# Optimization experiments

Hardware: AMD Instinct MI355X
Metric: run time of the kernel (lower is better)

Reference implementation:

```python
import jax, jax.numpy as jnp
import numpy as np

BL = 512
Q_DIM = K_DIM = V_DIM = 512
R = 2
C = Q_DIM // R  # 256


def setup_inputs() -> dict:
    key = jax.random.key(0)
    ks = jax.random.split(key, 11)
    L = 32768
    x1 = jax.random.normal(ks[0], (1, Q_DIM, L), dtype=jnp.float32)
    x2 = jax.random.normal(ks[1], (1, Q_DIM, L), dtype=jnp.float32)
    mask = jnp.ones((1, 1, L), dtype=jnp.float32)
    s_in = 1.0 / np.sqrt(Q_DIM)
    s_out = 1.0 / np.sqrt(C)
    Wq = jax.random.normal(ks[2], (C, Q_DIM), dtype=jnp.float32) * s_in
    bq = jax.random.normal(ks[3], (C,), dtype=jnp.float32) * 0.01
    Wk = jax.random.normal(ks[4], (C, K_DIM), dtype=jnp.float32) * s_in
    bk = jax.random.normal(ks[5], (C,), dtype=jnp.float32) * 0.01
    Wv = jax.random.normal(ks[6], (C, V_DIM), dtype=jnp.float32) * s_in
    bv = jax.random.normal(ks[7], (C,), dtype=jnp.float32) * 0.01
    Wo = jax.random.normal(ks[8], (V_DIM, C), dtype=jnp.float32) * s_out
    bo = jax.random.normal(ks[9], (V_DIM,), dtype=jnp.float32) * 0.01
    return {"x1": x1, "x2": x2, "mask": mask, "Wq": Wq, "bq": bq,
            "Wk": Wk, "bk": bk, "Wv": Wv, "bv": bv, "Wo": Wo, "bo": bo}


def _sliding_att(x1, mask, Wq, bq, Wk, bk, Wv, bv, Wo, bo):
    bl = BL
    half = bl // 2
    B, _, L = x1.shape  # B == 1 (asserted in original)
    # 1x1 Conv1d projections == per-position matmuls over channels
    q = jnp.einsum('oc,bcl->bol', Wq, x1) + bq[None, :, None]  # (1,C,L)
    k = jnp.einsum('oc,bcl->bol', Wk, x1) + bk[None, :, None]
    v = jnp.einsum('oc,bcl->bol', Wv, x1) + bv[None, :, None]
    c1 = q.shape[1]
    nb = L // bl  # L chosen as multiple of bl; padding branch is a no-op
    pm = mask[:, 0:1, :]  # (1,1,L)
    # query blocks: (nb, C, bl)
    qb = q.reshape(1, c1, nb, bl).transpose(0, 2, 1, 3).reshape(nb, c1, bl)
    # pad K/V/mask with bl//2 zeros each side, gather overlapping windows of width 2*bl
    k_pad = jnp.pad(k, ((0, 0), (0, 0), (half, half)))[0]      # (C, L+bl)
    v_pad = jnp.pad(v, ((0, 0), (0, 0), (half, half)))[0]
    pm_pad = jnp.pad(pm, ((0, 0), (0, 0), (half, half)))[0, 0]  # (L+bl,)
    idx = jnp.arange(nb)[:, None] * bl + jnp.arange(2 * bl)[None, :]  # (nb, 2bl)
    kw = k_pad[:, idx].transpose(1, 0, 2)  # (nb, C, 2bl)
    vw = v_pad[:, idx].transpose(1, 0, 2)  # (nb, C, 2bl)
    pmw = pm_pad[idx][:, None, :]          # (nb, 1, 2bl)
    # banded window mask: query i attends keys j with i <= j < i+bl (in window coords)
    rows = jnp.arange(bl)[:, None]
    cols = jnp.arange(2 * bl)[None, :]
    wmask = ((cols >= rows) & (cols < rows + bl)).astype(x1.dtype)  # (bl, 2bl)
    fmask = wmask[None, :, :] * pmw  # (nb, bl, 2bl)
    scale = 1.0 / np.sqrt(c1)
    energy = jnp.einsum('ncl,ncm->nlm', qb, kw) * scale  # (nb, bl, 2bl)
    attn = jax.nn.softmax(energy + jnp.log(fmask + 1e-6), axis=-1) * fmask
    out = jnp.einsum('ncm,nlm->ncl', vw, attn)  # (nb, C, bl)
    out = jax.nn.relu(out)
    out = jnp.einsum('oc,ncl->nol', Wo, out) + bo[None, :, None]  # (nb, V, bl)
    out = out[None].transpose(0, 2, 1, 3).reshape(1, Wo.shape[0], nb * bl)
    return out[:, :, :L] * pm


def reference(x1, x2, mask, Wq, bq, Wk, bk, Wv, bv, Wo, bo):
    # x2 is accepted by the original forward but unused in self-attention
    return _sliding_att(x1, mask, Wq, bq, Wk, bk, Wv, bv, Wo, bo)
```

## Files before the change

kernel.cpp:

```cpp
#include <hip/hip_runtime.h>
#include <hip/hip_bf16.h>
#include <math.h>

#define L 32768
#define C 256
#define QD 512
#define SCALE (1.0f/16.0f)

typedef __hip_bfloat16 bf16;
typedef short v8s __attribute__((ext_vector_type(8)));
typedef short v4s __attribute__((ext_vector_type(4)));
typedef float v4f __attribute__((ext_vector_type(4)));

__device__ __forceinline__ void ldst16(void* lds, const void* g) {
    __builtin_amdgcn_global_load_lds(
        (const __attribute__((address_space(1))) unsigned int*)g,
        (__attribute__((address_space(3))) unsigned int*)lds, 16, 0, 0);
}
__device__ __forceinline__ short bfbits(float x) {
    bf16 h = __float2bfloat16(x);
    return *reinterpret_cast<short*>(&h);
}

__global__ __launch_bounds__(256) void prep(
    const float* __restrict__ Wq, const float* __restrict__ Wk,
    const float* __restrict__ Wv, const float* __restrict__ bq,
    const float* __restrict__ bk, const float* __restrict__ bv,
    const float* __restrict__ Wo,
    bf16* __restrict__ Wall, bf16* __restrict__ Wob, float* __restrict__ ball)
{
    int i = blockIdx.x * 256 + threadIdx.x;
    if (i < 768*512) {
        int row = i >> 9, idx = i & 511;
        const float* src = row < 256 ? Wq : row < 512 ? Wk : Wv;
        Wall[i] = __float2bfloat16(src[(row & 255) * 512 + idx]);
    } else if (i < 768*512 + 512*256) {
        int j = i - 768*512;
        Wob[j] = __float2bfloat16(Wo[j]);
    } else if (i < 768*512 + 512*256 + 768) {
        int j = i - 768*512 - 512*256;
        ball[j] = j < 256 ? bq[j] : j < 512 ? bk[j - 256] : bv[j - 512];
    }
}

__global__ __launch_bounds__(256) void convt(
    const float* __restrict__ x, short* __restrict__ xT)
{
    __shared__ short st[64*72];
    const int t = threadIdx.x;
    const int l0 = blockIdx.x * 64, c0 = blockIdx.y * 64;
    #pragma unroll
    for (int i = 0; i < 2; i++) {
        int v = i*256 + t;
        int c = v >> 3, l8 = (v & 7) << 3;
        const float* p = x + (size_t)(c0 + c) * L + l0 + l8;
        float4 f0 = *(const float4*)p;
        float4 f1 = *(const float4*)(p + 4);
        bf16* stb = (bf16*)st;
        stb[(l8+0)*72 + c] = __float2bfloat16(f0.x);
        stb[(l8+1)*72 + c] = __float2bfloat16(f0.y);
        stb[(l8+2)*72 + c] = __float2bfloat16(f0.z);
        stb[(l8+3)*72 + c] = __float2bfloat16(f0.w);
        stb[(l8+4)*72 + c] = __float2bfloat16(f1.x);
        stb[(l8+5)*72 + c] = __float2bfloat16(f1.y);
        stb[(l8+6)*72 + c] = __float2bfloat16(f1.z);
        stb[(l8+7)*72 + c] = __float2bfloat16(f1.w);
    }
    __syncthreads();
    #pragma unroll
    for (int i = 0; i < 2; i++) {
        int v = i*256 + t;
        int l = v >> 3, c8 = (v & 7) << 3;
        *(v8s*)(xT + (size_t)(l0 + l) * QD + c0 + c8) = *(const v8s*)&st[l*72 + c8];
    }
}

__global__ __launch_bounds__(256) void qkv_gemm(
    const bf16* __restrict__ A, const bf16* __restrict__ B,
    const float* __restrict__ ball,
    bf16* __restrict__ qT, bf16* __restrict__ kT, bf16* __restrict__ vB)
{
    __shared__ short sA[128*32];
    __shared__ short sB[128*32];
    __shared__ short sE[128*136];

    const int t    = threadIdx.x;
    const int lane = t & 63;
    const int w    = t >> 6;
    const int wm   = w & 1, wn = w >> 1;
    const int col  = lane & 15, quad = lane >> 4;
    const int n0   = blockIdx.x * 128;
    const int my   = blockIdx.y;
    const int m0   = my * 128;

    v4f acc[4][4];
    #pragma unroll
    for (int i = 0; i < 4; i++)
        #pragma unroll
        for (int j = 0; j < 4; j++) acc[i][j] = (v4f){0.f,0.f,0.f,0.f};

    for (int k0 = 0; k0 < QD; k0 += 32) {
        #pragma unroll
        for (int j = 0; j < 2; j++) {
            int idx = j*256 + t;
            int m = idx >> 2, k8 = (idx & 3) << 3;
            ldst16(&sA[idx*8], A + (size_t)(m0 + m) * QD + k0 + k8);
        }
        #pragma unroll
        for (int j = 0; j < 2; j++) {
            int idx = j*256 + t;
            int n = idx >> 2, k8 = (idx & 3) << 3;
            ldst16(&sB[idx*8], B + (size_t)(n0 + n) * QD + k0 + k8);
        }
        __syncthreads();
        v8s af[4], bf[4];
        #pragma unroll
        for (int mt = 0; mt < 4; mt++)
            af[mt] = *(const v8s*)&sA[(wm*64 + mt*16 + col)*32 + quad*8];
        #pragma unroll
        for (int nt = 0; nt < 4; nt++)
            bf[nt] = *(const v8s*)&sB[(wn*64 + nt*16 + col)*32 + quad*8];
        #pragma unroll
        for (int mt = 0; mt < 4; mt++)
            #pragma unroll
            for (int nt = 0; nt < 4; nt++)
                acc[mt][nt] = __builtin_amdgcn_mfma_f32_16x16x32_bf16(af[mt], bf[nt], acc[mt][nt], 0, 0, 0);
        __syncthreads();
    }

    float bias_v[4][4];
    #pragma unroll
    for (int mt = 0; mt < 4; mt++)
        #pragma unroll
        for (int r = 0; r < 4; r++)
            bias_v[mt][r] = ball[m0 + wm*64 + mt*16 + quad*4 + r];

    bf16* sEb = (bf16*)sE;
    if (my < 4) {
        #pragma unroll
        for (int mt = 0; mt < 4; mt++)
            #pragma unroll
            for (int nt = 0; nt < 4; nt++)
                #pragma unroll
                for (int r = 0; r < 4; r++)
                    sEb[(wn*64 + nt*16 + col)*136 + wm*64 + mt*16 + quad*4 + r] =
                        __float2bfloat16(acc[mt][nt][r] + bias_v[mt][r]);
        __syncthreads();
        bf16* dst = (my < 2) ? qT : kT;
        const int c0 = (my & 1) * 128;
        #pragma unroll
        for (int j = 0; j < 8; j++) {
            int idx = j*256 + t;
            int n = idx >> 4, c8 = (idx & 15) << 3;
            *(v8s*)(dst + (size_t)(n0 + n) * C + c0 + c8) = *(const v8s*)&sE[n*136 + c8];
        }
    } else {
        #pragma unroll
        for (int mt = 0; mt < 4; mt++)
            #pragma unroll
            for (int nt = 0; nt < 4; nt++)
                #pragma unroll
                for (int r = 0; r < 4; r++)
                    sEb[(wm*64 + mt*16 + quad*4 + r)*136 + wn*64 + nt*16 + col] =
                        __float2bfloat16(acc[mt][nt][r] + bias_v[mt][r]);
        __syncthreads();
        const int c0 = (my - 4) * 128;
        #pragma unroll
        for (int j = 0; j < 8; j++) {
            int idx = j*256 + t;
            int m = idx >> 4, n8 = (idx & 15) << 3;
            *(v8s*)(vB + (size_t)(c0 + m) * L + n0 + n8) = *(const v8s*)&sE[m*136 + n8];
        }
    }
}

__global__ __launch_bounds__(256) void out_gemm(
    const bf16* __restrict__ A, const bf16* __restrict__ B,
    const float* __restrict__ bo, const float* __restrict__ mask,
    float* __restrict__ out)
{
    __shared__ short sA[128*32];
    __shared__ short sB[128*32];

    const int t    = threadIdx.x;
    const int lane = t & 63;
    const int w    = t >> 6;
    const int wm   = w & 1, wn = w >> 1;
    const int col  = lane & 15, quad = lane >> 4;
    const int n0   = blockIdx.x * 128;
    const int m0   = blockIdx.y * 128;

    v4f acc[4][4];
    #pragma unroll
    for (int i = 0; i < 4; i++)
        #pragma unroll
        for (int j = 0; j < 4; j++) acc[i][j] = (v4f){0.f,0.f,0.f,0.f};

    for (int k0 = 0; k0 < C; k0 += 32) {
        #pragma unroll
        for (int j = 0; j < 2; j++) {
            int idx = j*256 + t;
            int m = idx >> 2, k8 = (idx & 3) << 3;
            ldst16(&sA[idx*8], A + (size_t)(m0 + m) * C + k0 + k8);
        }
        #pragma unroll
        for (int j = 0; j < 2; j++) {
            int idx = j*256 + t;
            int n = idx >> 2, k8 = (idx & 3) << 3;
            ldst16(&sB[idx*8], B + (size_t)(n0 + n) * C + k0 + k8);
        }
        __syncthreads();
        v8s af[4], bf[4];
        #pragma unroll
        for (int mt = 0; mt < 4; mt++)
            af[mt] = *(const v8s*)&sA[(wm*64 + mt*16 + col)*32 + quad*8];
        #pragma unroll
        for (int nt = 0; nt < 4; nt++)
            bf[nt] = *(const v8s*)&sB[(wn*64 + nt*16 + col)*32 + quad*8];
        #pragma unroll
        for (int mt = 0; mt < 4; mt++)
            #pragma unroll
            for (int nt = 0; nt < 4; nt++)
                acc[mt][nt] = __builtin_amdgcn_mfma_f32_16x16x32_bf16(af[mt], bf[nt], acc[mt][nt], 0, 0, 0);
        __syncthreads();
    }

    float bias_v[4];
    #pragma unroll
    for (int mt = 0; mt < 4; mt++)
        bias_v[mt] = 0.f;
    #pragma unroll
    for (int mt = 0; mt < 4; mt++) {
        #pragma unroll
        for (int r = 0; r < 4; r++) {
            int m = m0 + wm*64 + mt*16 + quad*4 + r;
            float bb = bo[m];
            #pragma unroll
            for (int nt = 0; nt < 4; nt++) {
                int n = n0 + wn*64 + nt*16 + col;
                out[(size_t)m * L + n] = (acc[mt][nt][r] + bb) * mask[n];
            }
        }
    }
}

__global__ __launch_bounds__(256, 2) void attn_mfma(
    const bf16* __restrict__ qT, const bf16* __restrict__ kT,
    const bf16* __restrict__ vB, const float* __restrict__ mask,
    bf16* __restrict__ aoT)
{
    __shared__ short sK [64*264];
    __shared__ short sVt[256*72];
    __shared__ short sP [4][16*72];

    const int t    = threadIdx.x;
    const int w    = t >> 6;
    const int lane = t & 63;
    const int col  = lane & 15;
    const int quad = lane >> 4;
    const int p0   = blockIdx.x * 64;
    const int abase = p0 - 256;

    v8s qf[8];
    {
        const short* qp = (const short*)qT + (size_t)(p0 + w*16 + col) * C + quad*8;
        #pragma unroll
        for (int ks = 0; ks < 8; ks++) qf[ks] = *(const v8s*)(qp + ks*32);
    }

    v4f oacc[16];
    #pragma unroll
    for (int i = 0; i < 16; i++) oacc[i] = (v4f){0.f, 0.f, 0.f, 0.f};
    float mrow[4] = {-1e30f, -1e30f, -1e30f, -1e30f};
    float lrow[4] = {0.f, 0.f, 0.f, 0.f};

    for (int ch = 0; ch < 9; ch++) {
        const int a0 = abase + ch*64;
        __syncthreads();
        #pragma unroll
        for (int i = 0; i < 8; i++) {
            int idx = i*256 + t;
            int r = idx >> 5, cb = (idx & 31) << 3;
            int a = a0 + r;
            v8s val = {0,0,0,0,0,0,0,0};
            if (a >= 0 && a < L)
                val = *(const v8s*)((const short*)kT + (size_t)a * C + cb);
            *(v8s*)&sK[r*264 + cb] = val;
        }
        if (a0 >= 0 && a0 + 63 < L) {
            #pragma unroll
            for (int i = 0; i < 8; i++) {
                int idx = i*256 + t;
                int c = idx >> 3, kb = (idx & 7) << 3;
                *(v8s*)&sVt[c*72 + kb] =
                    *(const v8s*)((const short*)vB + (size_t)c * L + a0 + kb);
            }
        } else {
            #pragma unroll
            for (int i = 0; i < 8; i++) {
                int idx = i*256 + t;
                int c = idx >> 3, kb = (idx & 7) << 3;
                v8s val;
                #pragma unroll
                for (int j = 0; j < 8; j++) {
                    int a = a0 + kb + j;
                    val[j] = (a >= 0 && a < L)
                        ? ((const short*)vB)[(size_t)c * L + a] : (short)0;
                }
                *(v8s*)&sVt[c*72 + kb] = val;
            }
        }
        __syncthreads();

        v4f e[4];
        #pragma unroll
        for (int nt = 0; nt < 4; nt++) {
            v4f acc = {0.f, 0.f, 0.f, 0.f};
            const short* kp = &sK[(nt*16 + col)*264 + quad*8];
            #pragma unroll
            for (int ks = 0; ks < 8; ks++) {
                v8s bfrag = *(const v8s*)(kp + ks*32);
                acc = __builtin_amdgcn_mfma_f32_16x16x32_bf16(qf[ks], bfrag, acc, 0, 0, 0);
            }
            e[nt] = acc;
        }

        float cmax[4] = {-1e30f, -1e30f, -1e30f, -1e30f};
        #pragma unroll
        for (int nt = 0; nt < 4; nt++) {
            int a  = a0 + nt*16 + col;
            int aa = ch*64 + nt*16 + col;
            float mval = (a >= 0 && a < L) ? mask[a] : 0.f;
            #pragma unroll
            for (int r = 0; r < 4; r++) {
                int rel = aa - (w*16 + quad*4 + r);
                bool valid = ((unsigned)rel < 512u) && (mval > 0.f);
                float ev = valid ? e[nt][r] * SCALE : -1e30f;
                e[nt][r] = ev;
                cmax[r] = fmaxf(cmax[r], ev);
            }
        }
        #pragma unroll
        for (int off = 1; off < 16; off <<= 1) {
            #pragma unroll
            for (int r = 0; r < 4; r++)
                cmax[r] = fmaxf(cmax[r], __shfl_xor(cmax[r], off));
        }

        float alpha[4];
        #pragma unroll
        for (int r = 0; r < 4; r++) {
            float mnew = fmaxf(mrow[r], cmax[r]);
            alpha[r] = __expf(mrow[r] - mnew);
            mrow[r] = mnew;
        }

        float psum[4] = {0.f, 0.f, 0.f, 0.f};
        bf16* sPw = (bf16*)sP[w];
        #pragma unroll
        for (int nt = 0; nt < 4; nt++) {
            #pragma unroll
            for (int r = 0; r < 4; r++) {
                float ev = e[nt][r];
                float p = (ev > -9e29f) ? __expf(ev - mrow[r]) : 0.f;
                psum[r] += p;
                sPw[(quad*4 + r)*72 + nt*16 + col] = __float2bfloat16(p);
            }
        }
        #pragma unroll
        for (int off = 1; off < 16; off <<= 1) {
            #pragma unroll
            for (int r = 0; r < 4; r++)
                psum[r] += __shfl_xor(psum[r], off);
        }
        #pragma unroll
        for (int r = 0; r < 4; r++) lrow[r] = lrow[r]*alpha[r] + psum[r];

        {
            int src = (col >> 2) << 4;
            float a0b = __shfl(alpha[0], src);
            float a1b = __shfl(alpha[1], src);
            float a2b = __shfl(alpha[2], src);
            float a3b = __shfl(alpha[3], src);
            int rr = col & 3;
            float aO = (rr == 0) ? a0b : (rr == 1) ? a1b : (rr == 2) ? a2b : a3b;
            #pragma unroll
            for (int i = 0; i < 16; i++) {
                oacc[i][0] *= aO; oacc[i][1] *= aO;
                oacc[i][2] *= aO; oacc[i][3] *= aO;
            }
        }

        {
            const short* sPws = (const short*)sP[w];
            v8s pf0 = *(const v8s*)&sPws[col*72 + quad*8];
            v8s pf1 = *(const v8s*)&sPws[col*72 + quad*8 + 32];
            #pragma unroll
            for (int ct = 0; ct < 16; ct++) {
                const short* vp = &sVt[(ct*16 + col)*72 + quad*8];
                v8s vf0 = *(const v8s*)vp;
                v8s vf1 = *(const v8s*)(vp + 32);
                oacc[ct] = __builtin_amdgcn_mfma_f32_16x16x32_bf16(vf0, pf0, oacc[ct], 0, 0, 0);
                oacc[ct] = __builtin_amdgcn_mfma_f32_16x16x32_bf16(vf1, pf1, oacc[ct], 0, 0, 0);
            }
        }
    }

    {
        int src = (col >> 2) << 4;
        float l0b = __shfl(lrow[0], src);
        float l1b = __shfl(lrow[1], src);
        float l2b = __shfl(lrow[2], src);
        float l3b = __shfl(lrow[3], src);
        int rr = col & 3;
        float lO = (rr == 0) ? l0b : (rr == 1) ? l1b : (rr == 2) ? l2b : l3b;
        float inv = (lO > 0.f) ? 1.f / lO : 0.f;
        const int qg = p0 + w*16 + col;
        short* aorow = (short*)aoT + (size_t)qg * C;
        #pragma unroll
        for (int ct = 0; ct < 16; ct++) {
            v4s pk;
            #pragma unroll
            for (int r = 0; r < 4; r++)
                pk[r] = bfbits(fmaxf(oacc[ct][r] * inv, 0.f));
            *(v4s*)(aorow + ct*16 + quad*4) = pk;
        }
    }
}

extern "C" void kernel_launch(void* const* d_in, const int* in_sizes, int n_in,
                              void* d_out, int out_size, void* d_ws, size_t ws_size,
                              hipStream_t stream)
{
    const float* x1   = (const float*)d_in[0];
    const float* mask = (const float*)d_in[2];
    const float* Wq   = (const float*)d_in[3];
    const float* bq   = (const float*)d_in[4];
    const float* Wk   = (const float*)d_in[5];
    const float* bk   = (const float*)d_in[6];
    const float* Wv   = (const float*)d_in[7];
    const float* bv   = (const float*)d_in[8];
    const float* Wo   = (const float*)d_in[9];
    const float* bo   = (const float*)d_in[10];
    float* out = (float*)d_out;

    bf16* x1T  = (bf16*)d_ws;
    bf16* Wall = x1T + (size_t)L * QD;
    bf16* Wob  = Wall + 768*512;
    float* ball = (float*)(Wob + 512*256);
    bf16* qT   = (bf16*)(ball + 768);
    bf16* kT   = qT + (size_t)L * C;
    bf16* vB   = kT + (size_t)L * C;
    bf16* aoT  = vB + (size_t)L * C;

    dim3 blk(256);
    prep<<<dim3((768*512 + 512*256 + 768 + 255)/256), blk, 0, stream>>>(
        Wq, Wk, Wv, bq, bk, bv, Wo, Wall, Wob, ball);
    convt<<<dim3(L/64, QD/64), blk, 0, stream>>>(x1, (short*)x1T);
    qkv_gemm<<<dim3(L/128, 6), blk, 0, stream>>>(Wall, x1T, ball, qT, kT, vB);
    attn_mfma<<<dim3(L/64), blk, 0, stream>>>(qT, kT, vB, mask, aoT);
    out_gemm<<<dim3(L/128, 4), blk, 0, stream>>>(Wob, aoT, bo, mask, out);
}
```

Measured before the change: 304.5 us.

## Double-buffer K/V loads via registers, widen attention tile, coalesce output stores

The attention kernel now uses 512 threads covering 128 queries per block, so each streamed K/V chunk serves twice as many queries and there are fewer redundant window loads (10 chunks per 128 queries instead of 9 per 64). The next chunk is prefetched into registers while the current one is computed, then written to LDS, which hides global load latency. Block indices are swizzled to change tile ordering. The output GEMM epilogue stages results through shared memory to emit coalesced float4 stores with vectorized mask loads. The costs are extra register pressure from the prefetch buffers and extra LDS use and barriers in out_gemm.

```diff
diff --git a/kernel.cpp b/kernel.cpp
--- a/kernel.cpp
+++ b/kernel.cpp
@@ -181,6 +181,7 @@
 {
     __shared__ short sA[128*32];
     __shared__ short sB[128*32];
+    __shared__ float sEf[64*132];
 
     const int t    = threadIdx.x;
     const int lane = t & 63;
@@ -225,40 +226,106 @@
         __syncthreads();
     }
 
-    float bias_v[4];
-    #pragma unroll
-    for (int mt = 0; mt < 4; mt++)
-        bias_v[mt] = 0.f;
-    #pragma unroll
-    for (int mt = 0; mt < 4; mt++) {
-        #pragma unroll
-        for (int r = 0; r < 4; r++) {
-            int m = m0 + wm*64 + mt*16 + quad*4 + r;
-            float bb = bo[m];
-            #pragma unroll
-            for (int nt = 0; nt < 4; nt++) {
-                int n = n0 + wn*64 + nt*16 + col;
-                out[(size_t)m * L + n] = (acc[mt][nt][r] + bb) * mask[n];
-            }
-        }
-    }
-}
-
-__global__ __launch_bounds__(256, 2) void attn_mfma(
+    #pragma unroll
+    for (int half = 0; half < 2; half++) {
+        if (wm == half) {
+            #pragma unroll
+            for (int mt = 0; mt < 4; mt++) {
+                #pragma unroll
+                for (int r = 0; r < 4; r++) {
+                    float bb = bo[m0 + half*64 + mt*16 + quad*4 + r];
+                    #pragma unroll
+                    for (int nt = 0; nt < 4; nt++)
+                        sEf[(mt*16 + quad*4 + r)*132 + wn*64 + nt*16 + col] =
+                            acc[mt][nt][r] + bb;
+                }
+            }
+        }
+        __syncthreads();
+        #pragma unroll
+        for (int j = 0; j < 8; j++) {
+            int idx = j*256 + t;
+            int row = idx >> 5, s4 = (idx & 31) << 2;
+            float4 vv = *(const float4*)&sEf[row*132 + s4];
+            float4 mk = *(const float4*)&mask[n0 + s4];
+            vv.x *= mk.x; vv.y *= mk.y; vv.z *= mk.z; vv.w *= mk.w;
+            *(float4*)&out[(size_t)(m0 + half*64 + row) * L + n0 + s4] = vv;
+        }
+        __syncthreads();
+    }
+}
+
+__device__ __forceinline__ void load_chunk(
+    const short* __restrict__ kT, const short* __restrict__ vB,
+    int a0, int t, v8s kreg[4], v8s vreg[4])
+{
+    #pragma unroll
+    for (int j = 0; j < 4; j++) {
+        int idx = j*512 + t;
+        int r = idx >> 5, s = idx & 31;
+        int a = a0 + r;
+        v8s kv = {0,0,0,0,0,0,0,0};
+        if (a >= 0 && a < L) kv = *(const v8s*)(kT + (size_t)a * C + s*8);
+        kreg[j] = kv;
+    }
+    if (a0 >= 0 && a0 + 63 < L) {
+        #pragma unroll
+        for (int j = 0; j < 4; j++) {
+            int idx = j*512 + t;
+            int c = idx >> 3, s = idx & 7;
+            vreg[j] = *(const v8s*)(vB + (size_t)c * L + a0 + s*8);
+        }
+    } else {
+        #pragma unroll
+        for (int j = 0; j < 4; j++) {
+            int idx = j*512 + t;
+            int c = idx >> 3, s = idx & 7;
+            v8s val;
+            #pragma unroll
+            for (int e2 = 0; e2 < 8; e2++) {
+                int a = a0 + s*8 + e2;
+                val[e2] = (a >= 0 && a < L) ? vB[(size_t)c * L + a] : (short)0;
+            }
+            vreg[j] = val;
+        }
+    }
+}
+
+__device__ __forceinline__ void store_chunk(
+    short* __restrict__ sK, short* __restrict__ sVt, int t,
+    const v8s kreg[4], const v8s vreg[4])
+{
+    #pragma unroll
+    for (int j = 0; j < 4; j++) {
+        int idx = j*512 + t;
+        int r = idx >> 5, s = idx & 31;
+        *(v8s*)&sK[r*264 + s*8] = kreg[j];
+    }
+    #pragma unroll
+    for (int j = 0; j < 4; j++) {
+        int idx = j*512 + t;
+        int c = idx >> 3, s = idx & 7;
+        *(v8s*)&sVt[c*72 + s*8] = vreg[j];
+    }
+}
+
+__global__ __launch_bounds__(512, 2) void attn_mfma(
     const bf16* __restrict__ qT, const bf16* __restrict__ kT,
     const bf16* __restrict__ vB, const float* __restrict__ mask,
     bf16* __restrict__ aoT)
 {
     __shared__ short sK [64*264];
     __shared__ short sVt[256*72];
-    __shared__ short sP [4][16*72];
+    __shared__ short sP [8][16*72];
 
     const int t    = threadIdx.x;
     const int w    = t >> 6;
     const int lane = t & 63;
     const int col  = lane & 15;
     const int quad = lane >> 4;
-    const int p0   = blockIdx.x * 64;
+    const int bx   = blockIdx.x;
+    const int tile = ((bx & 7) << 5) | (bx >> 3);
+    const int p0   = tile * 128;
     const int abase = p0 - 256;
 
     v8s qf[8];
@@ -274,43 +341,16 @@
     float mrow[4] = {-1e30f, -1e30f, -1e30f, -1e30f};
     float lrow[4] = {0.f, 0.f, 0.f, 0.f};
 
-    for (int ch = 0; ch < 9; ch++) {
+    v8s kreg[4], vreg[4];
+    load_chunk((const short*)kT, (const short*)vB, abase, t, kreg, vreg);
+    store_chunk(sK, sVt, t, kreg, vreg);
+    __syncthreads();
+
+    for (int ch = 0; ch < 10; ch++) {
         const int a0 = abase + ch*64;
-        __syncthreads();
-        #pragma unroll
-        for (int i = 0; i < 8; i++) {
-            int idx = i*256 + t;
-            int r = idx >> 5, cb = (idx & 31) << 3;
-            int a = a0 + r;
-            v8s val = {0,0,0,0,0,0,0,0};
-            if (a >= 0 && a < L)
-                val = *(const v8s*)((const short*)kT + (size_t)a * C + cb);
-            *(v8s*)&sK[r*264 + cb] = val;
-        }
-        if (a0 >= 0 && a0 + 63 < L) {
-            #pragma unroll
-            for (int i = 0; i < 8; i++) {
-                int idx = i*256 + t;
-                int c = idx >> 3, kb = (idx & 7) << 3;
-                *(v8s*)&sVt[c*72 + kb] =
-                    *(const v8s*)((const short*)vB + (size_t)c * L + a0 + kb);
-            }
-        } else {
-            #pragma unroll
-            for (int i = 0; i < 8; i++) {
-                int idx = i*256 + t;
-                int c = idx >> 3, kb = (idx & 7) << 3;
-                v8s val;
-                #pragma unroll
-                for (int j = 0; j < 8; j++) {
-                    int a = a0 + kb + j;
-                    val[j] = (a >= 0 && a < L)
-                        ? ((const short*)vB)[(size_t)c * L + a] : (short)0;
-                }
-                *(v8s*)&sVt[c*72 + kb] = val;
-            }
-        }
-        __syncthreads();
+        const bool pf = (ch < 9);
+        if (pf)
+            load_chunk((const short*)kT, (const short*)vB, a0 + 64, t, kreg, vreg);
 
         v4f e[4];
         #pragma unroll
@@ -403,6 +443,12 @@
                 oacc[ct] = __builtin_amdgcn_mfma_f32_16x16x32_bf16(vf0, pf0, oacc[ct], 0, 0, 0);
                 oacc[ct] = __builtin_amdgcn_mfma_f32_16x16x32_bf16(vf1, pf1, oacc[ct], 0, 0, 0);
             }
+        }
+
+        if (pf) {
+            __syncthreads();
+            store_chunk(sK, sVt, t, kreg, vreg);
+            __syncthreads();
         }
     }
 
@@ -458,6 +504,6 @@
         Wq, Wk, Wv, bq, bk, bv, Wo, Wall, Wob, ball);
     convt<<<dim3(L/64, QD/64), blk, 0, stream>>>(x1, (short*)x1T);
     qkv_gemm<<<dim3(L/128, 6), blk, 0, stream>>>(Wall, x1T, ball, qT, kT, vB);
-    attn_mfma<<<dim3(L/64), blk, 0, stream>>>(qT, kT, vB, mask, aoT);
+    attn_mfma<<<dim3(L/128), dim3(512), 0, stream>>>(qT, kT, vB, mask, aoT);
     out_gemm<<<dim3(L/128, 4), blk, 0, stream>>>(Wob, aoT, bo, mask, out);
 }
```

New measurement: 292.0 us. 1.04x faster.

## Load K/V fragments directly from global in attention and stage output GEMM stores through LDS

Applied to the files above, without the earlier changes.

The attention kernel stops staging K and V chunks in shared memory. Each wave now reads MFMA fragments straight from global memory, with clamped indices so boundary rows stay in bounds and masking handles validity. This removes two block barriers per chunk and raises the occupancy hint to 3, and block indices are remapped so neighbouring tiles run apart. The output GEMM epilogue writes results into an LDS buffer and then emits coalesced float4 stores with the mask applied. The cost is redundant global and L2 traffic, since all four waves fetch the same K/V data.

```diff
diff --git a/kernel.cpp b/kernel.cpp
--- a/kernel.cpp
+++ b/kernel.cpp
@@ -181,6 +181,7 @@
 {
     __shared__ short sA[128*32];
     __shared__ short sB[128*32];
+    __shared__ float sEf[64*132];
 
     const int t    = threadIdx.x;
     const int lane = t & 63;
@@ -225,40 +226,50 @@
         __syncthreads();
     }
 
-    float bias_v[4];
-    #pragma unroll
-    for (int mt = 0; mt < 4; mt++)
-        bias_v[mt] = 0.f;
-    #pragma unroll
-    for (int mt = 0; mt < 4; mt++) {
-        #pragma unroll
-        for (int r = 0; r < 4; r++) {
-            int m = m0 + wm*64 + mt*16 + quad*4 + r;
-            float bb = bo[m];
-            #pragma unroll
-            for (int nt = 0; nt < 4; nt++) {
-                int n = n0 + wn*64 + nt*16 + col;
-                out[(size_t)m * L + n] = (acc[mt][nt][r] + bb) * mask[n];
-            }
-        }
-    }
-}
-
-__global__ __launch_bounds__(256, 2) void attn_mfma(
+    #pragma unroll
+    for (int half = 0; half < 2; half++) {
+        if (wm == half) {
+            #pragma unroll
+            for (int mt = 0; mt < 4; mt++) {
+                #pragma unroll
+                for (int r = 0; r < 4; r++) {
+                    float bb = bo[m0 + half*64 + mt*16 + quad*4 + r];
+                    #pragma unroll
+                    for (int nt = 0; nt < 4; nt++)
+                        sEf[(mt*16 + quad*4 + r)*132 + wn*64 + nt*16 + col] =
+                            acc[mt][nt][r] + bb;
+                }
+            }
+        }
+        __syncthreads();
+        #pragma unroll
+        for (int j = 0; j < 8; j++) {
+            int idx = j*256 + t;
+            int row = idx >> 5, s4 = (idx & 31) << 2;
+            float4 vv = *(const float4*)&sEf[row*132 + s4];
+            float4 mk = *(const float4*)&mask[n0 + s4];
+            vv.x *= mk.x; vv.y *= mk.y; vv.z *= mk.z; vv.w *= mk.w;
+            *(float4*)&out[(size_t)(m0 + half*64 + row) * L + n0 + s4] = vv;
+        }
+        __syncthreads();
+    }
+}
+
+__global__ __launch_bounds__(256, 3) void attn_mfma(
     const bf16* __restrict__ qT, const bf16* __restrict__ kT,
     const bf16* __restrict__ vB, const float* __restrict__ mask,
     bf16* __restrict__ aoT)
 {
-    __shared__ short sK [64*264];
-    __shared__ short sVt[256*72];
-    __shared__ short sP [4][16*72];
+    __shared__ short sP[4][16*72];
 
     const int t    = threadIdx.x;
     const int w    = t >> 6;
     const int lane = t & 63;
     const int col  = lane & 15;
     const int quad = lane >> 4;
-    const int p0   = blockIdx.x * 64;
+    const int bx   = blockIdx.x;
+    const int tile = ((bx & 7) << 6) | (bx >> 3);
+    const int p0   = tile * 64;
     const int abase = p0 - 256;
 
     v8s qf[8];
@@ -274,49 +285,21 @@
     float mrow[4] = {-1e30f, -1e30f, -1e30f, -1e30f};
     float lrow[4] = {0.f, 0.f, 0.f, 0.f};
 
+    const short* kTs = (const short*)kT;
+    const short* vBs = (const short*)vB;
+    bf16* sPw  = (bf16*)sP[w];
+    const short* sPws = (const short*)sP[w];
+
     for (int ch = 0; ch < 9; ch++) {
         const int a0 = abase + ch*64;
-        __syncthreads();
-        #pragma unroll
-        for (int i = 0; i < 8; i++) {
-            int idx = i*256 + t;
-            int r = idx >> 5, cb = (idx & 31) << 3;
-            int a = a0 + r;
-            v8s val = {0,0,0,0,0,0,0,0};
-            if (a >= 0 && a < L)
-                val = *(const v8s*)((const short*)kT + (size_t)a * C + cb);
-            *(v8s*)&sK[r*264 + cb] = val;
-        }
-        if (a0 >= 0 && a0 + 63 < L) {
-            #pragma unroll
-            for (int i = 0; i < 8; i++) {
-                int idx = i*256 + t;
-                int c = idx >> 3, kb = (idx & 7) << 3;
-                *(v8s*)&sVt[c*72 + kb] =
-                    *(const v8s*)((const short*)vB + (size_t)c * L + a0 + kb);
-            }
-        } else {
-            #pragma unroll
-            for (int i = 0; i < 8; i++) {
-                int idx = i*256 + t;
-                int c = idx >> 3, kb = (idx & 7) << 3;
-                v8s val;
-                #pragma unroll
-                for (int j = 0; j < 8; j++) {
-                    int a = a0 + kb + j;
-                    val[j] = (a >= 0 && a < L)
-                        ? ((const short*)vB)[(size_t)c * L + a] : (short)0;
-                }
-                *(v8s*)&sVt[c*72 + kb] = val;
-            }
-        }
-        __syncthreads();
 
         v4f e[4];
         #pragma unroll
         for (int nt = 0; nt < 4; nt++) {
+            int a  = a0 + nt*16 + col;
+            int ac = min(max(a, 0), L - 1);
+            const short* kp = kTs + (size_t)ac * C + quad*8;
             v4f acc = {0.f, 0.f, 0.f, 0.f};
-            const short* kp = &sK[(nt*16 + col)*264 + quad*8];
             #pragma unroll
             for (int ks = 0; ks < 8; ks++) {
                 v8s bfrag = *(const v8s*)(kp + ks*32);
@@ -356,7 +339,6 @@
         }
 
         float psum[4] = {0.f, 0.f, 0.f, 0.f};
-        bf16* sPw = (bf16*)sP[w];
         #pragma unroll
         for (int nt = 0; nt < 4; nt++) {
             #pragma unroll
@@ -392,14 +374,17 @@
         }
 
         {
-            const short* sPws = (const short*)sP[w];
             v8s pf0 = *(const v8s*)&sPws[col*72 + quad*8];
             v8s pf1 = *(const v8s*)&sPws[col*72 + quad*8 + 32];
+            int ag0 = a0 + quad*8;
+            int ag1 = a0 + 32 + quad*8;
+            int ac0 = min(max(ag0, 0), L - 8);
+            int ac1 = min(max(ag1, 0), L - 8);
             #pragma unroll
             for (int ct = 0; ct < 16; ct++) {
-                const short* vp = &sVt[(ct*16 + col)*72 + quad*8];
-                v8s vf0 = *(const v8s*)vp;
-                v8s vf1 = *(const v8s*)(vp + 32);
+                const short* vrow = vBs + (size_t)(ct*16 + col) * L;
+                v8s vf0 = *(const v8s*)(vrow + ac0);
+                v8s vf1 = *(const v8s*)(vrow + ac1);
                 oacc[ct] = __builtin_amdgcn_mfma_f32_16x16x32_bf16(vf0, pf0, oacc[ct], 0, 0, 0);
                 oacc[ct] = __builtin_amdgcn_mfma_f32_16x16x32_bf16(vf1, pf1, oacc[ct], 0, 0, 0);
             }
```

Result: slower. 411.5 us (+35.1%).
